# Kernel optimization log

Hardware: AMD Instinct MI355X
Metric: run time of the kernel (lower is better)

## Reference

```python
import jax, jax.numpy as jnp
import numpy as np

N_NODES = 50000
N_EDGES = 800000
D_FEAT = 128
N_HEADS = 4
HEAD_DIM = 32  # embed_dim 128 / 4 heads


def mish(x):
    return x * jnp.tanh(jax.nn.softplus(x))


def setup_inputs() -> dict:
    key = jax.random.key(0)
    ks = jax.random.split(key, 12)
    s = 1.0 / np.sqrt(D_FEAT)
    return {
        "nodes": jax.random.normal(ks[0], (N_NODES, D_FEAT), jnp.float32),
        "edges": jax.random.normal(ks[1], (N_EDGES, D_FEAT), jnp.float32),
        # DenseGeneral kernels [in, heads, head_dim], biases [heads, head_dim]
        "Ws_k": jax.random.normal(ks[2], (D_FEAT, N_HEADS, HEAD_DIM), jnp.float32) * s,
        "Ws_b": jnp.zeros((N_HEADS, HEAD_DIM), jnp.float32),
        "Wr_k": jax.random.normal(ks[3], (D_FEAT, N_HEADS, HEAD_DIM), jnp.float32) * s,
        "Wr_b": jnp.zeros((N_HEADS, HEAD_DIM), jnp.float32),
        "We_k": jax.random.normal(ks[4], (D_FEAT, N_HEADS, HEAD_DIM), jnp.float32) * s,
        "We_b": jnp.zeros((N_HEADS, HEAD_DIM), jnp.float32),
        # attention logit Dense(1): acts on last (head_dim) axis
        "attn_w": jax.random.normal(ks[5], (HEAD_DIM, 1), jnp.float32) / np.sqrt(HEAD_DIM),
        "attn_b": jnp.zeros((1,), jnp.float32),
        "senders": jax.random.randint(ks[6], (N_EDGES,), 0, N_NODES, jnp.int32),
        "receivers": jax.random.randint(ks[7], (N_EDGES,), 0, N_NODES, jnp.int32),
    }


def reference(nodes, edges, Ws_k, Ws_b, Wr_k, Wr_b, We_k, We_b, attn_w, attn_b,
              senders, receivers):
    n = nodes.shape[0]
    # update_edge_fn: W_s(nodes[senders]) + W_e(edges)   (no globals -> 0)
    sent = jnp.einsum('ef,fhd->ehd', nodes[senders], Ws_k) + Ws_b       # [E,H,D]
    e_att = sent + jnp.einsum('ef,fhd->ehd', edges, We_k) + We_b        # [E,H,D]
    # attention_logit_fn: Dense1(mish(edges + W_r(nodes[receivers])))
    recv = jnp.einsum('ef,fhd->ehd', nodes[receivers], Wr_k) + Wr_b     # [E,H,D]
    logits = jnp.einsum('ehd,do->eho', mish(e_att + recv), attn_w) + attn_b  # [E,H,1]
    # jraph.segment_softmax over receiver segments
    seg_max = jax.ops.segment_max(logits, receivers, num_segments=n)
    w = jnp.exp(logits - seg_max[receivers])
    denom = jax.ops.segment_sum(w, receivers, num_segments=n)
    w = w / denom[receivers]
    # attention_reduce_fn + segment_sum aggregation; node update = aggregated msgs
    msg = (w * e_att).reshape(e_att.shape[0], N_HEADS * HEAD_DIM)       # [E, H*D]
    out_nodes = jax.ops.segment_sum(msg, receivers, num_segments=n)     # [N, H*D]
    return out_nodes
```

## Files before the change

### kernel.cpp

```cpp
#include <hip/hip_runtime.h>
#include <hip/hip_bf16.h>

#define NN 50000
#define NE 800000
#define F 128
#define HD 128
#define H 4

typedef __attribute__((ext_vector_type(4))) float f32x4;
typedef __attribute__((ext_vector_type(8))) __bf16 bf16x8;


__device__ __forceinline__ float mish_f(float x) {
    if (x > 30.f) return x;
    float t = __expf(x);
    float u = 1.f + t;
    u = u * u;
    return x * (u - 1.f) * __builtin_amdgcn_rcpf(u + 1.f);
}

__device__ __forceinline__ unsigned f32_to_bf16(float x) {
    unsigned u = __float_as_uint(x);
    u += 0x7FFFu + ((u >> 16) & 1u);
    return u >> 16;
}
__device__ __forceinline__ float bf16lo_to_f32(unsigned p) {
    return __uint_as_float((p & 0xFFFFu) << 16);
}
__device__ __forceinline__ float bf16hi_to_f32(unsigned p) {
    return __uint_as_float(p & 0xFFFF0000u);
}

__global__ __launch_bounds__(256) void prep_w(
    const float* __restrict__ W0, const float* __restrict__ W1,
    const float* __restrict__ W2, uint4* __restrict__ O)
{
    int b = blockIdx.x;
    const float* W = (b == 0) ? W0 : (b == 1) ? W1 : W2;
    uint4* out = O + b * 2048;
    for (int c = threadIdx.x; c < 2048; c += 256) {
        int fn = c >> 8, ks = (c >> 6) & 3, lane = c & 63;
        int lgp = lane >> 4, l15 = lane & 15;
        int col = fn * 16 + l15, k0 = ks * 32 + lgp * 8;
        unsigned u[4];
        #pragma unroll
        for (int i = 0; i < 4; ++i) {
            float a = W[(k0 + 2 * i) * 128 + col];
            float bb = W[(k0 + 2 * i + 1) * 128 + col];
            u[i] = f32_to_bf16(a) | (f32_to_bf16(bb) << 16);
        }
        out[c] = make_uint4(u[0], u[1], u[2], u[3]);
    }
}

__global__ __launch_bounds__(256) void hist_kernel(
    const int* __restrict__ receivers, unsigned* __restrict__ cnt)
{
    int i = blockIdx.x * 256 + threadIdx.x;
    if (i < NE) atomicAdd(&cnt[receivers[i]], 1u);
}

__global__ __launch_bounds__(256) void scan1_kernel(
    const unsigned* __restrict__ cnt, unsigned* __restrict__ rowptr,
    unsigned* __restrict__ bsum)
{
    __shared__ unsigned sh[256];
    const int t = threadIdx.x;
    int i = blockIdx.x * 256 + t;
    unsigned c = (i < NN) ? cnt[i] : 0u;
    sh[t] = c;
    __syncthreads();
    unsigned incl = c;
    for (int off = 1; off < 256; off <<= 1) {
        unsigned v = (t >= off) ? sh[t - off] : 0u;
        __syncthreads();
        incl += v;
        sh[t] = incl;
        __syncthreads();
    }
    if (i < NN) rowptr[i] = incl - c;
    if (t == 255) bsum[blockIdx.x] = incl;
}

__global__ __launch_bounds__(256) void scan2_kernel(
    unsigned* __restrict__ bsum, unsigned* __restrict__ boff, int nb,
    unsigned* __restrict__ rowptr)
{
    __shared__ unsigned sh[256];
    const int t = threadIdx.x;
    unsigned c = (t < nb) ? bsum[t] : 0u;
    sh[t] = c;
    __syncthreads();
    unsigned incl = c;
    for (int off = 1; off < 256; off <<= 1) {
        unsigned v = (t >= off) ? sh[t - off] : 0u;
        __syncthreads();
        incl += v;
        sh[t] = incl;
        __syncthreads();
    }
    if (t < nb) boff[t] = incl - c;
    if (t == 0) rowptr[NN] = NE;
}

__global__ __launch_bounds__(256) void scan3_kernel(
    unsigned* __restrict__ rowptr, const unsigned* __restrict__ boff)
{
    int i = blockIdx.x * 256 + threadIdx.x;
    if (i < NN) rowptr[i] += boff[blockIdx.x];
}

__global__ __launch_bounds__(256) void scatter_kernel(
    const int* __restrict__ receivers, const unsigned* __restrict__ rowptr,
    unsigned* __restrict__ cnt2, unsigned* __restrict__ jof)
{
    int i = blockIdx.x * 256 + threadIdx.x;
    if (i >= NE) return;
    int r = receivers[i];
    unsigned pos = rowptr[r] + atomicAdd(&cnt2[r], 1u);
    jof[i] = pos;
}

__global__ __launch_bounds__(256, 4) void proj_both(
    const float* __restrict__ X,
    const bf16x8* __restrict__ Wf0, const bf16x8* __restrict__ Wf1,
    const float* __restrict__ b0, const float* __restrict__ b1,
    int M, uint2* __restrict__ Sp, uint2* __restrict__ Rp)
{
    __shared__ __align__(16) char ldsA[32768];
    const int t = threadIdx.x;
    const int lane = t & 63;
    const int wid = t >> 6;
    const int wr = wid >> 1, wc = wid & 1;
    const int l15 = lane & 15, lgp = lane >> 4;
    const size_t rowbase = (size_t)blockIdx.x * 128;

    #pragma unroll
    for (int i = 0; i < 8; ++i) {
        int c = i * 256 + t;
        int row = c >> 4, cc = c & 15;
        size_t e = rowbase + row;
        uint4 p = make_uint4(0, 0, 0, 0);
        if (e < (size_t)M) {
            const float4* src = (const float4*)(X + e * F + cc * 8);
            float4 f0 = src[0], f1 = src[1];
            p.x = f32_to_bf16(f0.x) | (f32_to_bf16(f0.y) << 16);
            p.y = f32_to_bf16(f0.z) | (f32_to_bf16(f0.w) << 16);
            p.z = f32_to_bf16(f1.x) | (f32_to_bf16(f1.y) << 16);
            p.w = f32_to_bf16(f1.z) | (f32_to_bf16(f1.w) << 16);
        }
        unsigned byte = (unsigned)(row * 256 + cc * 16);
        byte ^= (unsigned)((row & 7) << 4);
        *(uint4*)(ldsA + byte) = p;
    }
    __syncthreads();

    #pragma unroll
    for (int pass = 0; pass < 2; ++pass) {
        const bf16x8* Wf = pass ? Wf1 : Wf0;
        const float* bias = pass ? b1 : b0;
        uint2* Y = pass ? Rp : Sp;

        f32x4 acc[4][4];
        #pragma unroll
        for (int n = 0; n < 4; ++n) {
            float bv = bias[wc * 64 + n * 16 + l15];
            #pragma unroll
            for (int m = 0; m < 4; ++m) {
                acc[m][n][0] = bv; acc[m][n][1] = bv;
                acc[m][n][2] = bv; acc[m][n][3] = bv;
            }
        }
        #pragma unroll
        for (int ks = 0; ks < 4; ++ks) {
            const int kb = ks * 64 + lgp * 16;
            bf16x8 af[4], bfr[4];
            #pragma unroll
            for (int m = 0; m < 4; ++m) {
                int row = wr * 64 + m * 16 + l15;
                unsigned byte = ((unsigned)(row * 256 + kb)) ^ ((row & 7) << 4);
                af[m] = *(const bf16x8*)(ldsA + byte);
            }
            #pragma unroll
            for (int n = 0; n < 4; ++n)
                bfr[n] = Wf[((wc * 4 + n) * 4 + ks) * 64 + lane];
            #pragma unroll
            for (int m = 0; m < 4; ++m)
                #pragma unroll
                for (int n = 0; n < 4; ++n)
                    acc[m][n] = __builtin_amdgcn_mfma_f32_16x16x32_bf16(
                        af[m], bfr[n], acc[m][n], 0, 0, 0);
        }
        #pragma unroll
        for (int m = 0; m < 4; ++m)
            #pragma unroll
            for (int j = 0; j < 4; ++j) {
                int row = wr * 64 + m * 16 + lgp * 4 + j;
                size_t e = rowbase + row;
                if (e >= (size_t)M) continue;
                uint2 pk;
                pk.x = f32_to_bf16(acc[m][0][j]) | (f32_to_bf16(acc[m][1][j]) << 16);
                pk.y = f32_to_bf16(acc[m][2][j]) | (f32_to_bf16(acc[m][3][j]) << 16);
                Y[e * 32 + l15 * 2 + wc] = pk;
            }
    }
}

__global__ __launch_bounds__(256, 8) void edge_gemm(
    const float* __restrict__ X, const bf16x8* __restrict__ Wf,
    const float* __restrict__ bias,
    const int* __restrict__ senders, const unsigned* __restrict__ jof,
    const uint4* __restrict__ Sp4, uint4* __restrict__ EAp)
{
    __shared__ __align__(16) char ldsA[16384];
    const int t = threadIdx.x;
    const int lane = t & 63;
    const int wid = t >> 6;
    const int l15 = lane & 15, lgp = lane >> 4;
    const size_t rowbase = (size_t)blockIdx.x * 64;

    #pragma unroll
    for (int i = 0; i < 4; ++i) {
        int c = i * 256 + t;
        int row = c >> 4, cc = c & 15;
        const float4* src = (const float4*)(X + (rowbase + row) * F + cc * 8);
        float4 f0 = src[0], f1 = src[1];
        uint4 p;
        p.x = f32_to_bf16(f0.x) | (f32_to_bf16(f0.y) << 16);
        p.y = f32_to_bf16(f0.z) | (f32_to_bf16(f0.w) << 16);
        p.z = f32_to_bf16(f1.x) | (f32_to_bf16(f1.y) << 16);
        p.w = f32_to_bf16(f1.z) | (f32_to_bf16(f1.w) << 16);
        unsigned byte = (unsigned)(row * 256 + cc * 16);
        byte ^= (unsigned)((row & 7) << 4);
        *(uint4*)(ldsA + byte) = p;
    }

    f32x4 acc[8];
    #pragma unroll
    for (int n = 0; n < 8; ++n) {
        float bv = bias[n * 16 + l15];
        acc[n][0] = bv; acc[n][1] = bv; acc[n][2] = bv; acc[n][3] = bv;
    }
    __syncthreads();

    #pragma unroll
    for (int ks = 0; ks < 4; ++ks) {
        int arow = wid * 16 + l15;
        unsigned abyte = ((unsigned)(arow * 256 + ks * 64 + lgp * 16))
                         ^ ((arow & 7) << 4);
        bf16x8 af = *(const bf16x8*)(ldsA + abyte);
        #pragma unroll
        for (int n = 0; n < 8; ++n) {
            bf16x8 bfr = Wf[(n * 4 + ks) * 64 + lane];
            acc[n] = __builtin_amdgcn_mfma_f32_16x16x32_bf16(af, bfr, acc[n], 0, 0, 0);
        }
    }

    #pragma unroll
    for (int j = 0; j < 4; ++j) {
        int row = wid * 16 + lgp * 4 + j;
        size_t e = rowbase + row;
        int snd = senders[e];
        unsigned jj = jof[e];
        uint4 sv = Sp4[(size_t)snd * 16 + l15];
        unsigned uo[4];
        #pragma unroll
        for (int h = 0; h < 4; ++h) {
            unsigned sp = (h == 0) ? sv.x : (h == 1) ? sv.y : (h == 2) ? sv.z : sv.w;
            float elo = acc[2 * h][j]     + bf16lo_to_f32(sp);
            float ehi = acc[2 * h + 1][j] + bf16hi_to_f32(sp);
            uo[h] = f32_to_bf16(elo) | (f32_to_bf16(ehi) << 16);
        }
        EAp[(size_t)jj * 16 + l15] = make_uint4(uo[0], uo[1], uo[2], uo[3]);
    }
}

__global__ __launch_bounds__(256) void agg_kernel(
    const unsigned* __restrict__ rowptr,
    const uint4* __restrict__ Rp4,
    const float* __restrict__ attw, const float* __restrict__ attb,
    const unsigned* __restrict__ EA, float* __restrict__ out)
{
    const int lane = threadIdx.x & 63;
    const int r = blockIdx.x * 4 + (threadIdx.x >> 6);
    if (r >= NN) return;
    const unsigned start = rowptr[r], end = rowptr[r + 1];

    const int h    = lane & 3;
    const int l15c = lane >> 2;
    const int c0   = 32 * h + l15c;

    if (start == end) {
        out[(size_t)r * HD + c0]      = 0.f;
        out[(size_t)r * HD + c0 + 16] = 0.f;
        return;
    }

    uint4 rv4 = Rp4[(size_t)r * 16 + l15c];
    unsigned rp = (h == 0) ? rv4.x : (h == 1) ? rv4.y : (h == 2) ? rv4.z : rv4.w;
    const float rlo = bf16lo_to_f32(rp), rhi = bf16hi_to_f32(rp);
    const float aw0 = attw[l15c];
    const float aw1 = attw[l15c + 16];
    const float ab0 = attb[0];
    const unsigned* ea = EA + lane;

    float ax0 = 0.f, ay0 = 0.f, dn0 = 0.f;
    float ax1 = 0.f, ay1 = 0.f, dn1 = 0.f;
    unsigned j = start;
    for (; j + 2 <= end; j += 2) {
        unsigned p0 = ea[(size_t)j * 64];
        unsigned p1 = ea[(size_t)(j + 1) * 64];
        float e0l = bf16lo_to_f32(p0), e0h = bf16hi_to_f32(p0);
        float e1l = bf16lo_to_f32(p1), e1h = bf16hi_to_f32(p1);
        float t0 = mish_f(e0l + rlo) * aw0 + mish_f(e0h + rhi) * aw1;
        float t1 = mish_f(e1l + rlo) * aw0 + mish_f(e1h + rhi) * aw1;
        t0 += __shfl_xor(t0, 4);   t1 += __shfl_xor(t1, 4);
        t0 += __shfl_xor(t0, 8);   t1 += __shfl_xor(t1, 8);
        t0 += __shfl_xor(t0, 16);  t1 += __shfl_xor(t1, 16);
        t0 += __shfl_xor(t0, 32);  t1 += __shfl_xor(t1, 32);
        float w0 = __expf(t0 + ab0);
        float w1 = __expf(t1 + ab0);
        dn0 += w0;  ax0 += w0 * e0l;  ay0 += w0 * e0h;
        dn1 += w1;  ax1 += w1 * e1l;  ay1 += w1 * e1h;
    }
    if (j < end) {
        unsigned p0 = ea[(size_t)j * 64];
        float e0l = bf16lo_to_f32(p0), e0h = bf16hi_to_f32(p0);
        float t0 = mish_f(e0l + rlo) * aw0 + mish_f(e0h + rhi) * aw1;
        t0 += __shfl_xor(t0, 4);
        t0 += __shfl_xor(t0, 8);
        t0 += __shfl_xor(t0, 16);
        t0 += __shfl_xor(t0, 32);
        float w0 = __expf(t0 + ab0);
        dn0 += w0;  ax0 += w0 * e0l;  ay0 += w0 * e0h;
    }
    float rd = 1.f / (dn0 + dn1);
    out[(size_t)r * HD + c0]      = (ax0 + ax1) * rd;
    out[(size_t)r * HD + c0 + 16] = (ay0 + ay1) * rd;
}

extern "C" void kernel_launch(void* const* d_in, const int* in_sizes, int n_in,
                              void* d_out, int out_size, void* d_ws, size_t ws_size,
                              hipStream_t stream) {
    const float* nodes = (const float*)d_in[0];
    const float* edges = (const float*)d_in[1];
    const float* Ws_k  = (const float*)d_in[2];
    const float* Ws_b  = (const float*)d_in[3];
    const float* Wr_k  = (const float*)d_in[4];
    const float* Wr_b  = (const float*)d_in[5];
    const float* We_k  = (const float*)d_in[6];
    const float* We_b  = (const float*)d_in[7];
    const float* attw  = (const float*)d_in[8];
    const float* attb  = (const float*)d_in[9];
    const int* senders   = (const int*)d_in[10];
    const int* receivers = (const int*)d_in[11];
    float* out = (float*)d_out;

    char* ws = (char*)d_ws;
    const size_t CNT_OFF  = 0;
    const size_t CNT2_OFF = 200000;
    const size_t RP_OFF   = 400000;
    const size_t BS_OFF   = 600004;
    const size_t JOF_OFF  = 700000;
    const size_t WF_OFF   = 3900000;
    const size_t SP_OFF   = 4000000;
    const size_t RPP_OFF  = 16800000;
    const size_t EA_OFF   = 29600000;

    unsigned* cnt    = (unsigned*)(ws + CNT_OFF);
    unsigned* cnt2   = (unsigned*)(ws + CNT2_OFF);
    unsigned* rowptr = (unsigned*)(ws + RP_OFF);
    unsigned* bsum   = (unsigned*)(ws + BS_OFF);
    unsigned* boff   = bsum + 256;
    unsigned* jof    = (unsigned*)(ws + JOF_OFF);
    uint4*    Wf     = (uint4*)(ws + WF_OFF);
    uint2*    Sp     = (uint2*)(ws + SP_OFF);
    uint2*    Rp     = (uint2*)(ws + RPP_OFF);
    unsigned* EA     = (unsigned*)(ws + EA_OFF);
    (void)ws_size;

    const int NB = (NN + 255) / 256;

    prep_w<<<3, 256, 0, stream>>>(Ws_k, Wr_k, We_k, Wf);

    hipMemsetAsync(ws + CNT_OFF, 0, 400000, stream);
    hist_kernel<<<(NE + 255) / 256, 256, 0, stream>>>(receivers, cnt);
    scan1_kernel<<<NB, 256, 0, stream>>>(cnt, rowptr, bsum);
    scan2_kernel<<<1, 256, 0, stream>>>(bsum, boff, NB, rowptr);
    scan3_kernel<<<NB, 256, 0, stream>>>(rowptr, boff);
    scatter_kernel<<<(NE + 255) / 256, 256, 0, stream>>>(receivers, rowptr, cnt2, jof);

    proj_both<<<(NN + 127) / 128, 256, 0, stream>>>(
        nodes, (const bf16x8*)Wf, (const bf16x8*)(Wf + 2048),
        Ws_b, Wr_b, NN, Sp, Rp);

    edge_gemm<<<NE / 64, 256, 0, stream>>>(
        edges, (const bf16x8*)(Wf + 4096), We_b,
        senders, jof, (const uint4*)Sp, (uint4*)EA);

    agg_kernel<<<(NN + 3) / 4, 256, 0, stream>>>(
        rowptr, (const uint4*)Rp, attw, attb, EA, out);
}
```

Before: 363.2 us.

## Restructure aggregation to 16 lanes per node, fuse scans and memset, use native bf16 packing

The aggregation kernel now maps one 16-lane group to each receiver node, with each lane loading a full uint4 (all 4 heads) per edge, so a wave covers four nodes instead of one. This shortens the shuffle reductions and issues wider loads. The scan2 and scan3 passes are merged into one kernel that recomputes the block offset itself, and the counter memset is folded into the weight-prep launch. Manual bf16 rounding is replaced by native __bf16 conversions. Risks: lower per-node parallelism for high-degree nodes, and load imbalance between the groups inside a wave.

```diff
diff --git a/kernel.cpp b/kernel.cpp
--- a/kernel.cpp
+++ b/kernel.cpp
@@ -9,6 +9,7 @@
 
 typedef __attribute__((ext_vector_type(4))) float f32x4;
 typedef __attribute__((ext_vector_type(8))) __bf16 bf16x8;
+typedef __attribute__((ext_vector_type(2))) __bf16 bf16x2;
 
 
 __device__ __forceinline__ float mish_f(float x) {
@@ -19,10 +20,11 @@
     return x * (u - 1.f) * __builtin_amdgcn_rcpf(u + 1.f);
 }
 
-__device__ __forceinline__ unsigned f32_to_bf16(float x) {
-    unsigned u = __float_as_uint(x);
-    u += 0x7FFFu + ((u >> 16) & 1u);
-    return u >> 16;
+__device__ __forceinline__ unsigned pack2_bf16(float a, float b) {
+    bf16x2 v;
+    v.x = (__bf16)a;
+    v.y = (__bf16)b;
+    return __builtin_bit_cast(unsigned, v);
 }
 __device__ __forceinline__ float bf16lo_to_f32(unsigned p) {
     return __uint_as_float((p & 0xFFFFu) << 16);
@@ -33,9 +35,15 @@
 
 __global__ __launch_bounds__(256) void prep_w(
     const float* __restrict__ W0, const float* __restrict__ W1,
-    const float* __restrict__ W2, uint4* __restrict__ O)
+    const float* __restrict__ W2, uint4* __restrict__ O,
+    uint4* __restrict__ zero_dst)
 {
     int b = blockIdx.x;
+    if (b >= 3) {
+        int i = (b - 3) * 256 + threadIdx.x;
+        if (i < 25000) zero_dst[i] = make_uint4(0, 0, 0, 0);
+        return;
+    }
     const float* W = (b == 0) ? W0 : (b == 1) ? W1 : W2;
     uint4* out = O + b * 2048;
     for (int c = threadIdx.x; c < 2048; c += 256) {
@@ -44,11 +52,9 @@
         int col = fn * 16 + l15, k0 = ks * 32 + lgp * 8;
         unsigned u[4];
         #pragma unroll
-        for (int i = 0; i < 4; ++i) {
-            float a = W[(k0 + 2 * i) * 128 + col];
-            float bb = W[(k0 + 2 * i + 1) * 128 + col];
-            u[i] = f32_to_bf16(a) | (f32_to_bf16(bb) << 16);
-        }
+        for (int i = 0; i < 4; ++i)
+            u[i] = pack2_bf16(W[(k0 + 2 * i) * 128 + col],
+                              W[(k0 + 2 * i + 1) * 128 + col]);
         out[c] = make_uint4(u[0], u[1], u[2], u[3]);
     }
 }
@@ -82,11 +88,11 @@
     if (t == 255) bsum[blockIdx.x] = incl;
 }
 
-__global__ __launch_bounds__(256) void scan2_kernel(
-    unsigned* __restrict__ bsum, unsigned* __restrict__ boff, int nb,
-    unsigned* __restrict__ rowptr)
+__global__ __launch_bounds__(256) void scan3_kernel(
+    unsigned* __restrict__ rowptr, const unsigned* __restrict__ bsum, int nb)
 {
     __shared__ unsigned sh[256];
+    __shared__ unsigned s_off;
     const int t = threadIdx.x;
     unsigned c = (t < nb) ? bsum[t] : 0u;
     sh[t] = c;
@@ -99,15 +105,13 @@
         sh[t] = incl;
         __syncthreads();
     }
-    if (t < nb) boff[t] = incl - c;
-    if (t == 0) rowptr[NN] = NE;
-}
-
-__global__ __launch_bounds__(256) void scan3_kernel(
-    unsigned* __restrict__ rowptr, const unsigned* __restrict__ boff)
-{
-    int i = blockIdx.x * 256 + threadIdx.x;
-    if (i < NN) rowptr[i] += boff[blockIdx.x];
+    if (t == 0) {
+        s_off = (blockIdx.x > 0) ? sh[blockIdx.x - 1] : 0u;
+        if (blockIdx.x == 0) rowptr[NN] = NE;
+    }
+    __syncthreads();
+    int i = blockIdx.x * 256 + t;
+    if (i < NN) rowptr[i] += s_off;
 }
 
 __global__ __launch_bounds__(256) void scatter_kernel(
@@ -144,10 +148,10 @@
         if (e < (size_t)M) {
             const float4* src = (const float4*)(X + e * F + cc * 8);
             float4 f0 = src[0], f1 = src[1];
-            p.x = f32_to_bf16(f0.x) | (f32_to_bf16(f0.y) << 16);
-            p.y = f32_to_bf16(f0.z) | (f32_to_bf16(f0.w) << 16);
-            p.z = f32_to_bf16(f1.x) | (f32_to_bf16(f1.y) << 16);
-            p.w = f32_to_bf16(f1.z) | (f32_to_bf16(f1.w) << 16);
+            p.x = pack2_bf16(f0.x, f0.y);
+            p.y = pack2_bf16(f0.z, f0.w);
+            p.z = pack2_bf16(f1.x, f1.y);
+            p.w = pack2_bf16(f1.z, f1.w);
         }
         unsigned byte = (unsigned)(row * 256 + cc * 16);
         byte ^= (unsigned)((row & 7) << 4);
@@ -199,8 +203,8 @@
                 size_t e = rowbase + row;
                 if (e >= (size_t)M) continue;
                 uint2 pk;
-                pk.x = f32_to_bf16(acc[m][0][j]) | (f32_to_bf16(acc[m][1][j]) << 16);
-                pk.y = f32_to_bf16(acc[m][2][j]) | (f32_to_bf16(acc[m][3][j]) << 16);
+                pk.x = pack2_bf16(acc[m][0][j], acc[m][1][j]);
+                pk.y = pack2_bf16(acc[m][2][j], acc[m][3][j]);
                 Y[e * 32 + l15 * 2 + wc] = pk;
             }
     }
@@ -226,10 +230,10 @@
         const float4* src = (const float4*)(X + (rowbase + row) * F + cc * 8);
         float4 f0 = src[0], f1 = src[1];
         uint4 p;
-        p.x = f32_to_bf16(f0.x) | (f32_to_bf16(f0.y) << 16);
-        p.y = f32_to_bf16(f0.z) | (f32_to_bf16(f0.w) << 16);
-        p.z = f32_to_bf16(f1.x) | (f32_to_bf16(f1.y) << 16);
-        p.w = f32_to_bf16(f1.z) | (f32_to_bf16(f1.w) << 16);
+        p.x = pack2_bf16(f0.x, f0.y);
+        p.y = pack2_bf16(f0.z, f0.w);
+        p.z = pack2_bf16(f1.x, f1.y);
+        p.w = pack2_bf16(f1.z, f1.w);
         unsigned byte = (unsigned)(row * 256 + cc * 16);
         byte ^= (unsigned)((row & 7) << 4);
         *(uint4*)(ldsA + byte) = p;
@@ -269,7 +273,7 @@
             unsigned sp = (h == 0) ? sv.x : (h == 1) ? sv.y : (h == 2) ? sv.z : sv.w;
             float elo = acc[2 * h][j]     + bf16lo_to_f32(sp);
             float ehi = acc[2 * h + 1][j] + bf16hi_to_f32(sp);
-            uo[h] = f32_to_bf16(elo) | (f32_to_bf16(ehi) << 16);
+            uo[h] = pack2_bf16(elo, ehi);
         }
         EAp[(size_t)jj * 16 + l15] = make_uint4(uo[0], uo[1], uo[2], uo[3]);
     }
@@ -279,64 +283,71 @@
     const unsigned* __restrict__ rowptr,
     const uint4* __restrict__ Rp4,
     const float* __restrict__ attw, const float* __restrict__ attb,
-    const unsigned* __restrict__ EA, float* __restrict__ out)
+    const uint4* __restrict__ EA4, float* __restrict__ out)
 {
     const int lane = threadIdx.x & 63;
-    const int r = blockIdx.x * 4 + (threadIdx.x >> 6);
+    const int wid  = threadIdx.x >> 6;
+    const int g    = lane >> 4;
+    const int q    = lane & 15;
+    const int r = blockIdx.x * 16 + wid * 4 + g;
     if (r >= NN) return;
     const unsigned start = rowptr[r], end = rowptr[r + 1];
-
-    const int h    = lane & 3;
-    const int l15c = lane >> 2;
-    const int c0   = 32 * h + l15c;
+    float* orow = out + (size_t)r * HD;
 
     if (start == end) {
-        out[(size_t)r * HD + c0]      = 0.f;
-        out[(size_t)r * HD + c0 + 16] = 0.f;
+        #pragma unroll
+        for (int h = 0; h < 4; ++h) {
+            orow[32 * h + q] = 0.f;
+            orow[32 * h + 16 + q] = 0.f;
+        }
         return;
     }
 
-    uint4 rv4 = Rp4[(size_t)r * 16 + l15c];
-    unsigned rp = (h == 0) ? rv4.x : (h == 1) ? rv4.y : (h == 2) ? rv4.z : rv4.w;
-    const float rlo = bf16lo_to_f32(rp), rhi = bf16hi_to_f32(rp);
-    const float aw0 = attw[l15c];
-    const float aw1 = attw[l15c + 16];
+    uint4 rv = Rp4[(size_t)r * 16 + q];
+    float rlo[4], rhi[4];
+    rlo[0] = bf16lo_to_f32(rv.x); rhi[0] = bf16hi_to_f32(rv.x);
+    rlo[1] = bf16lo_to_f32(rv.y); rhi[1] = bf16hi_to_f32(rv.y);
+    rlo[2] = bf16lo_to_f32(rv.z); rhi[2] = bf16hi_to_f32(rv.z);
+    rlo[3] = bf16lo_to_f32(rv.w); rhi[3] = bf16hi_to_f32(rv.w);
+    const float aw0 = attw[q];
+    const float aw1 = attw[q + 16];
     const float ab0 = attb[0];
-    const unsigned* ea = EA + lane;
-
-    float ax0 = 0.f, ay0 = 0.f, dn0 = 0.f;
-    float ax1 = 0.f, ay1 = 0.f, dn1 = 0.f;
-    unsigned j = start;
-    for (; j + 2 <= end; j += 2) {
-        unsigned p0 = ea[(size_t)j * 64];
-        unsigned p1 = ea[(size_t)(j + 1) * 64];
-        float e0l = bf16lo_to_f32(p0), e0h = bf16hi_to_f32(p0);
-        float e1l = bf16lo_to_f32(p1), e1h = bf16hi_to_f32(p1);
-        float t0 = mish_f(e0l + rlo) * aw0 + mish_f(e0h + rhi) * aw1;
-        float t1 = mish_f(e1l + rlo) * aw0 + mish_f(e1h + rhi) * aw1;
-        t0 += __shfl_xor(t0, 4);   t1 += __shfl_xor(t1, 4);
-        t0 += __shfl_xor(t0, 8);   t1 += __shfl_xor(t1, 8);
-        t0 += __shfl_xor(t0, 16);  t1 += __shfl_xor(t1, 16);
-        t0 += __shfl_xor(t0, 32);  t1 += __shfl_xor(t1, 32);
-        float w0 = __expf(t0 + ab0);
-        float w1 = __expf(t1 + ab0);
-        dn0 += w0;  ax0 += w0 * e0l;  ay0 += w0 * e0h;
-        dn1 += w1;  ax1 += w1 * e1l;  ay1 += w1 * e1h;
-    }
-    if (j < end) {
-        unsigned p0 = ea[(size_t)j * 64];
-        float e0l = bf16lo_to_f32(p0), e0h = bf16hi_to_f32(p0);
-        float t0 = mish_f(e0l + rlo) * aw0 + mish_f(e0h + rhi) * aw1;
-        t0 += __shfl_xor(t0, 4);
-        t0 += __shfl_xor(t0, 8);
-        t0 += __shfl_xor(t0, 16);
-        t0 += __shfl_xor(t0, 32);
-        float w0 = __expf(t0 + ab0);
-        dn0 += w0;  ax0 += w0 * e0l;  ay0 += w0 * e0h;
-    }
-    float rd = 1.f / (dn0 + dn1);
-    out[(size_t)r * HD + c0]      = (ax0 + ax1) * rd;
-    out[(size_t)r * HD + c0 + 16] = (ay0 + ay1) * rd;
+
+    float accl[4] = {0.f, 0.f, 0.f, 0.f};
+    float acch[4] = {0.f, 0.f, 0.f, 0.f};
+    float den[4]  = {0.f, 0.f, 0.f, 0.f};
+
+    for (unsigned j = start; j < end; ++j) {
+        uint4 p = EA4[(size_t)j * 16 + q];
+        float el[4], eh[4], tt[4];
+        el[0] = bf16lo_to_f32(p.x); eh[0] = bf16hi_to_f32(p.x);
+        el[1] = bf16lo_to_f32(p.y); eh[1] = bf16hi_to_f32(p.y);
+        el[2] = bf16lo_to_f32(p.z); eh[2] = bf16hi_to_f32(p.z);
+        el[3] = bf16lo_to_f32(p.w); eh[3] = bf16hi_to_f32(p.w);
+        #pragma unroll
+        for (int h = 0; h < 4; ++h)
+            tt[h] = mish_f(el[h] + rlo[h]) * aw0 + mish_f(eh[h] + rhi[h]) * aw1;
+        #pragma unroll
+        for (int o = 1; o < 16; o <<= 1) {
+            tt[0] += __shfl_xor(tt[0], o);
+            tt[1] += __shfl_xor(tt[1], o);
+            tt[2] += __shfl_xor(tt[2], o);
+            tt[3] += __shfl_xor(tt[3], o);
+        }
+        #pragma unroll
+        for (int h = 0; h < 4; ++h) {
+            float w = __expf(tt[h] + ab0);
+            den[h]  += w;
+            accl[h] += w * el[h];
+            acch[h] += w * eh[h];
+        }
+    }
+    #pragma unroll
+    for (int h = 0; h < 4; ++h) {
+        float rd = 1.f / den[h];
+        orow[32 * h + q]      = accl[h] * rd;
+        orow[32 * h + 16 + q] = acch[h] * rd;
+    }
 }
 
 extern "C" void kernel_launch(void* const* d_in, const int* in_sizes, int n_in,
@@ -371,7 +382,6 @@
     unsigned* cnt2   = (unsigned*)(ws + CNT2_OFF);
     unsigned* rowptr = (unsigned*)(ws + RP_OFF);
     unsigned* bsum   = (unsigned*)(ws + BS_OFF);
-    unsigned* boff   = bsum + 256;
     unsigned* jof    = (unsigned*)(ws + JOF_OFF);
     uint4*    Wf     = (uint4*)(ws + WF_OFF);
     uint2*    Sp     = (uint2*)(ws + SP_OFF);
@@ -381,13 +391,11 @@
 
     const int NB = (NN + 255) / 256;
 
-    prep_w<<<3, 256, 0, stream>>>(Ws_k, Wr_k, We_k, Wf);
-
-    hipMemsetAsync(ws + CNT_OFF, 0, 400000, stream);
+    prep_w<<<3 + 98, 256, 0, stream>>>(Ws_k, Wr_k, We_k, Wf, (uint4*)(ws + CNT_OFF));
+
     hist_kernel<<<(NE + 255) / 256, 256, 0, stream>>>(receivers, cnt);
     scan1_kernel<<<NB, 256, 0, stream>>>(cnt, rowptr, bsum);
-    scan2_kernel<<<1, 256, 0, stream>>>(bsum, boff, NB, rowptr);
-    scan3_kernel<<<NB, 256, 0, stream>>>(rowptr, boff);
+    scan3_kernel<<<NB, 256, 0, stream>>>(rowptr, bsum, NB);
     scatter_kernel<<<(NE + 255) / 256, 256, 0, stream>>>(receivers, rowptr, cnt2, jof);
 
     proj_both<<<(NN + 127) / 128, 256, 0, stream>>>(
@@ -398,6 +406,6 @@
         edges, (const bf16x8*)(Wf + 4096), We_b,
         senders, jof, (const uint4*)Sp, (uint4*)EA);
 
-    agg_kernel<<<(NN + 3) / 4, 256, 0, stream>>>(
-        rowptr, (const uint4*)Rp, attw, attb, EA, out);
-}
+    agg_kernel<<<(NN + 15) / 16, 256, 0, stream>>>(
+        rowptr, (const uint4*)Rp, attw, attb, (const uint4*)EA, out);
+}
```

After: 394.0 us. 8.5% more time.
